# Performance work log

Measured on AMD Instinct MI355X. Metric: run time of the kernel, lower is better.

The kernel has to match this reference:

```python
import jax, jax.numpy as jnp
import numpy as np

N_NODES = 100000
N_EDGES = 1600000
N_IN = 64
N_OUT = 64


def setup_inputs() -> dict:
    key = jax.random.key(0)
    k_x, k_w, k_src, k_dst, k_val = jax.random.split(key, 5)
    X = jax.random.normal(k_x, (N_NODES, N_IN), dtype=jnp.float32)
    # Xavier-uniform init of the GCN weight matrix
    limit = float(np.sqrt(6.0 / (N_IN + N_OUT)))
    W = jax.random.uniform(k_w, (N_IN, N_OUT), dtype=jnp.float32,
                           minval=-limit, maxval=limit)
    # Sparse adjacency A in COO form: out[dst] += val * h[src]
    edge_src = jax.random.randint(k_src, (N_EDGES,), 0, N_NODES, dtype=jnp.int32)
    edge_dst = jax.random.randint(k_dst, (N_EDGES,), 0, N_NODES, dtype=jnp.int32)
    # normalized adjacency values (e.g., 1/sqrt(d_i d_j)); use uniform(0,1)
    edge_val = jax.random.uniform(k_val, (N_EDGES,), dtype=jnp.float32)
    return {"X": X, "W": W, "edge_val": edge_val,
            "edge_src": edge_src, "edge_dst": edge_dst}


def reference(X, W, edge_val, edge_src, edge_dst):
    # dropout p=0.0 -> identity (eval-mode math)
    h = X @ W                                   # [N, n_out] feature transform
    msgs = h[edge_src] * edge_val[:, None]      # [E, n_out] gather + scale
    agg = jax.ops.segment_sum(msgs, edge_dst, num_segments=N_NODES)  # A @ h
    return jax.nn.relu(agg)
```

## Files before the change

kernel.cpp:

```cpp
#include <hip/hip_runtime.h>
#include <hip/hip_bf16.h>

#define N_NODES 100000
#define N_IN    64
#define N_OUT   64
#define N_EDGES 1600000

#define BSHIFT  7
#define NPB     128
#define NB      782
#define CAP     2560
#define P1_EPT  32
#define P1_EPB  (512 * P1_EPT)
#define P1_BLOCKS ((N_EDGES + P1_EPB - 1) / P1_EPB)
#define GEMM_BLOCKS ((N_NODES + 63) / 64)

__device__ inline unsigned short f2bf(float f) {
    __hip_bfloat16 b = __float2bfloat16(f);
    union { __hip_bfloat16 b; unsigned short u; } c; c.b = b; return c.u;
}

__global__ __launch_bounds__(512) void prep_kernel(
        const float* __restrict__ X, const float* __restrict__ W,
        unsigned short* __restrict__ h,
        const int* __restrict__ edge_src, const int* __restrict__ edge_dst,
        const float* __restrict__ edge_val,
        int* __restrict__ bucket_cursor, int2* __restrict__ staged) {
    __shared__ float Ws[N_IN * N_OUT];
    const int t = threadIdx.x;

    if (blockIdx.x >= P1_BLOCKS) {
        const int blk = blockIdx.x - P1_BLOCKS;
        for (int i = t * 4; i < N_IN * N_OUT; i += 512 * 4)
            *(float4*)&Ws[i] = *(const float4*)&W[i];
        __syncthreads();

        const int r0 = blk * 64 + (t >> 4) * 2;
        const int c0 = (t & 15) * 4;
        if (r0 >= N_NODES) return;

        float acc0[4] = {0.f, 0.f, 0.f, 0.f};
        float acc1[4] = {0.f, 0.f, 0.f, 0.f};
        const float* x0p = X + (size_t)r0 * N_IN;
        const float* x1p = x0p + N_IN;

#pragma unroll 4
        for (int k4 = 0; k4 < 16; ++k4) {
            const float4 x0 = *(const float4*)(x0p + k4 * 4);
            const float4 x1 = *(const float4*)(x1p + k4 * 4);
            const float xa0[4] = {x0.x, x0.y, x0.z, x0.w};
            const float xa1[4] = {x1.x, x1.y, x1.z, x1.w};
#pragma unroll
            for (int kk = 0; kk < 4; ++kk) {
                const float4 w = *(const float4*)&Ws[(k4 * 4 + kk) * N_OUT + c0];
                acc0[0] = fmaf(xa0[kk], w.x, acc0[0]);
                acc0[1] = fmaf(xa0[kk], w.y, acc0[1]);
                acc0[2] = fmaf(xa0[kk], w.z, acc0[2]);
                acc0[3] = fmaf(xa0[kk], w.w, acc0[3]);
                acc1[0] = fmaf(xa1[kk], w.x, acc1[0]);
                acc1[1] = fmaf(xa1[kk], w.y, acc1[1]);
                acc1[2] = fmaf(xa1[kk], w.z, acc1[2]);
                acc1[3] = fmaf(xa1[kk], w.w, acc1[3]);
            }
        }
        ushort4 s0 = {f2bf(acc0[0]), f2bf(acc0[1]), f2bf(acc0[2]), f2bf(acc0[3])};
        ushort4 s1 = {f2bf(acc1[0]), f2bf(acc1[1]), f2bf(acc1[2]), f2bf(acc1[3])};
        *(ushort4*)&h[(size_t)r0 * N_OUT + c0] = s0;
        *(ushort4*)&h[(size_t)(r0 + 1) * N_OUT + c0] = s1;
    } else {
        int* cnt  = (int*)Ws;
        int* base = cnt + NB;
        for (int i = t; i < NB; i += 512) cnt[i] = 0;
        __syncthreads();

        const int e0 = blockIdx.x * P1_EPB + t * P1_EPT;
        const bool act = (e0 + P1_EPT) <= N_EDGES;

        if (act) {
#pragma unroll
            for (int q = 0; q < P1_EPT / 4; ++q) {
                const int4 d4 = *(const int4*)(edge_dst + e0 + q * 4);
                atomicAdd(&cnt[d4.x >> BSHIFT], 1);
                atomicAdd(&cnt[d4.y >> BSHIFT], 1);
                atomicAdd(&cnt[d4.z >> BSHIFT], 1);
                atomicAdd(&cnt[d4.w >> BSHIFT], 1);
            }
        }
        __syncthreads();
        for (int i = t; i < NB; i += 512) {
            const int c = cnt[i];
            base[i] = c ? atomicAdd(&bucket_cursor[i], c) : 0;
            cnt[i] = 0;
        }
        __syncthreads();
        if (act) {
#pragma unroll
            for (int q = 0; q < P1_EPT / 4; ++q) {
                const int4 d4 = *(const int4*)(edge_dst + e0 + q * 4);
                const int4 s4 = *(const int4*)(edge_src + e0 + q * 4);
                const int4 v4 = *(const int4*)((const int*)edge_val + e0 + q * 4);
                const int da[4] = {d4.x, d4.y, d4.z, d4.w};
                const int sa[4] = {s4.x, s4.y, s4.z, s4.w};
                const int va[4] = {v4.x, v4.y, v4.z, v4.w};
#pragma unroll
                for (int j = 0; j < 4; ++j) {
                    const int d = da[j];
                    const int b = d >> BSHIFT;
                    const int r = atomicAdd(&cnt[b], 1);
                    const int pos = base[b] + r;
                    if (pos < CAP) {
                        int2 o;
                        o.x = sa[j] | ((d & (NPB - 1)) << 17);
                        o.y = va[j];
                        staged[(size_t)b * CAP + pos] = o;
                    }
                }
            }
        }
    }
}

__global__ __launch_bounds__(512) void sort_gather_kernel(
        const uint2* __restrict__ h64,
        const int2* __restrict__ staged,
        const int* __restrict__ bucket_cursor,
        float* __restrict__ out) {
    __shared__ int2 srt[CAP];
    __shared__ int  ncnt[NPB];
    __shared__ int  noff[NPB];
    const int t = threadIdx.x;
    const int b = blockIdx.x;
    const int cnt = min(bucket_cursor[b], CAP);
    const int2* bucket = staged + (size_t)b * CAP;

    if (t < NPB) ncnt[t] = 0;
    __syncthreads();
    for (int e = t; e < cnt; e += 512)
        atomicAdd(&ncnt[(unsigned)bucket[e].x >> 17], 1);
    __syncthreads();
    if (t < NPB) noff[t] = ncnt[t];
    __syncthreads();
    for (int d = 1; d < NPB; d <<= 1) {
        int x = 0;
        if (t < NPB && t >= d) x = noff[t - d];
        __syncthreads();
        if (t < NPB) noff[t] += x;
        __syncthreads();
    }
    if (t < NPB) {
        const int excl = noff[t] - ncnt[t];
        noff[t] = excl;
        ncnt[t] = excl;
    }
    __syncthreads();
    for (int e = t; e < cnt; e += 512) {
        const int2 p = bucket[e];
        const int node = (unsigned)p.x >> 17;
        const int pos = atomicAdd(&ncnt[node], 1);
        int2 o; o.x = p.x & 0x1FFFF; o.y = p.y;
        srt[pos] = o;
    }
    __syncthreads();

    const int w  = t >> 6;
    const int q  = (t >> 4) & 3;
    const int ql = t & 15;

#define EDGE4(p, hw, v)                                                     \
    do {                                                                    \
        a0 = fmaf(__uint_as_float((hw).x << 16), (v), a0);                  \
        a1 = fmaf(__uint_as_float((hw).x & 0xffff0000u), (v), a1);          \
        a2 = fmaf(__uint_as_float((hw).y << 16), (v), a2);                  \
        a3 = fmaf(__uint_as_float((hw).y & 0xffff0000u), (v), a3);          \
    } while (0)

    for (int nl = w * 16; nl < w * 16 + 16; ++nl) {
        const int node = b * NPB + nl;
        if (node >= N_NODES) break;
        const int s = noff[nl];
        const int e_end = ncnt[nl];

        float a0 = 0.f, a1 = 0.f, a2 = 0.f, a3 = 0.f;
        int e = s + q;
        for (; e + 4 < e_end; e += 8) {
            const int2 p0 = srt[e];
            const int2 p1 = srt[e + 4];
            const uint2 w0 = h64[(size_t)p0.x * 16 + ql];
            const uint2 w1 = h64[(size_t)p1.x * 16 + ql];
            const float v0 = __int_as_float(p0.y);
            const float v1 = __int_as_float(p1.y);
            EDGE4(p0, w0, v0);
            EDGE4(p1, w1, v1);
        }
        for (; e < e_end; e += 4) {
            const int2 p = srt[e];
            const uint2 w0 = h64[(size_t)p.x * 16 + ql];
            const float v = __int_as_float(p.y);
            EDGE4(p, w0, v);
        }
        a0 += __shfl_xor(a0, 16, 64); a0 += __shfl_xor(a0, 32, 64);
        a1 += __shfl_xor(a1, 16, 64); a1 += __shfl_xor(a1, 32, 64);
        a2 += __shfl_xor(a2, 16, 64); a2 += __shfl_xor(a2, 32, 64);
        a3 += __shfl_xor(a3, 16, 64); a3 += __shfl_xor(a3, 32, 64);
        if (q == 0) {
            float4 o;
            o.x = fmaxf(a0, 0.f);
            o.y = fmaxf(a1, 0.f);
            o.z = fmaxf(a2, 0.f);
            o.w = fmaxf(a3, 0.f);
            *(float4*)&out[(size_t)node * 64 + 4 * ql] = o;
        }
    }
#undef EDGE4
}

__global__ __launch_bounds__(256) void gemm_f32_kernel(const float* __restrict__ X,
                                                       const float* __restrict__ W,
                                                       float* __restrict__ h) {
    __shared__ float Ws[N_IN * N_OUT];
    for (int i = threadIdx.x * 4; i < N_IN * N_OUT; i += 256 * 4)
        *(float4*)&Ws[i] = *(const float4*)&W[i];
    __syncthreads();
    const int lane = threadIdx.x & 63;
    const int wid = threadIdx.x >> 6;
    for (int row = blockIdx.x * 4 + wid; row < N_NODES; row += gridDim.x * 4) {
        const float x = X[row * N_IN + lane];
        float acc = 0.0f;
#pragma unroll
        for (int k = 0; k < N_IN; ++k)
            acc = fmaf(__shfl(x, k), Ws[k * N_OUT + lane], acc);
        h[row * N_OUT + lane] = acc;
    }
}

__global__ __launch_bounds__(256) void scatter_kernel(const float* __restrict__ h,
                                                      const float* __restrict__ edge_val,
                                                      const int* __restrict__ edge_src,
                                                      const int* __restrict__ edge_dst,
                                                      float* __restrict__ out) {
    const int lane = threadIdx.x & 63;
    const int e = (int)((blockIdx.x * 256u + threadIdx.x) >> 6);
    if (e >= N_EDGES) return;
    const float m = h[(size_t)edge_src[e] * N_OUT + lane] * edge_val[e];
    atomicAdd(&out[(size_t)edge_dst[e] * N_OUT + lane], m);
}

__global__ __launch_bounds__(256) void relu_kernel(float* __restrict__ out, int n) {
    const int i = (int)(blockIdx.x * 256u + threadIdx.x) * 4;
    if (i + 3 < n) {
        float4 v = *(float4*)&out[i];
        v.x = fmaxf(v.x, 0.f); v.y = fmaxf(v.y, 0.f);
        v.z = fmaxf(v.z, 0.f); v.w = fmaxf(v.w, 0.f);
        *(float4*)&out[i] = v;
    }
}

extern "C" void kernel_launch(void* const* d_in, const int* in_sizes, int n_in,
                              void* d_out, int out_size, void* d_ws, size_t ws_size,
                              hipStream_t stream) {
    const float* X        = (const float*)d_in[0];
    const float* W        = (const float*)d_in[1];
    const float* edge_val = (const float*)d_in[2];
    const int*   edge_src = (const int*)d_in[3];
    const int*   edge_dst = (const int*)d_in[4];
    float*       out      = (float*)d_out;

    unsigned short* h   = (unsigned short*)d_ws;
    int2* staged        = (int2*)((char*)d_ws + (size_t)N_NODES * N_OUT * 2);
    int*  bucket_cursor = (int*)(staged + (size_t)NB * CAP);
    const size_t need = (size_t)((char*)(bucket_cursor + NB) - (char*)d_ws);

    if (ws_size >= need) {
        hipMemsetAsync(bucket_cursor, 0, NB * sizeof(int), stream);
        prep_kernel<<<P1_BLOCKS + GEMM_BLOCKS, 512, 0, stream>>>(
            X, W, h, edge_src, edge_dst, edge_val, bucket_cursor, staged);
        sort_gather_kernel<<<NB, 512, 0, stream>>>((const uint2*)h, staged,
                                                   bucket_cursor, out);
    } else {
        float* hf = (float*)d_ws;
        hipMemsetAsync(d_out, 0, (size_t)out_size * sizeof(float), stream);
        gemm_f32_kernel<<<25000, 256, 0, stream>>>(X, W, hf);
        const long long st = (long long)N_EDGES * 64;
        scatter_kernel<<<(int)((st + 255) / 256), 256, 0, stream>>>(
            hf, edge_val, edge_src, edge_dst, out);
        relu_kernel<<<(out_size / 4 + 255) / 256, 256, 0, stream>>>(out, out_size);
    }
}
```

Baseline: 174.2 us.

## Stage edges in shared memory by bucket before coalesced global scatter

The binning pass now does a local counting sort in LDS. It prefix-scans the per-bucket counts and places each edge's packed (src, dst-low, val) record into a shared buffer ordered by bucket. Each wavefront then copies contiguous bucket runs to the global staged array, replacing scattered 8-byte writes with mostly contiguous ones. Edges per thread are halved so a block's edges fit in LDS, at the cost of more blocks, more global cursor atomics, a ~100KB LDS footprint that limits occupancy, and extra scan barriers.

```diff
diff --git a/kernel.cpp b/kernel.cpp
--- a/kernel.cpp
+++ b/kernel.cpp
@@ -10,10 +10,18 @@
 #define NPB     128
 #define NB      782
 #define CAP     2560
-#define P1_EPT  32
+#define P1_EPT  16
 #define P1_EPB  (512 * P1_EPT)
 #define P1_BLOCKS ((N_EDGES + P1_EPB - 1) / P1_EPB)
 #define GEMM_BLOCKS ((N_NODES + 63) / 64)
+
+#define SMEM_BYTES 100480
+#define OFF_SED   0
+#define OFF_LSCAN 65536
+#define OFF_CNT   69632
+#define OFF_GBASE 72760
+#define OFF_BKT   75888
+#define OFF_DLOW  92272
 
 __device__ inline unsigned short f2bf(float f) {
     __hip_bfloat16 b = __float2bfloat16(f);
@@ -26,10 +34,11 @@
         const int* __restrict__ edge_src, const int* __restrict__ edge_dst,
         const float* __restrict__ edge_val,
         int* __restrict__ bucket_cursor, int2* __restrict__ staged) {
-    __shared__ float Ws[N_IN * N_OUT];
+    __shared__ __align__(16) char smem[SMEM_BYTES];
     const int t = threadIdx.x;
 
     if (blockIdx.x >= P1_BLOCKS) {
+        float* Ws = (float*)smem;
         const int blk = blockIdx.x - P1_BLOCKS;
         for (int i = t * 4; i < N_IN * N_OUT; i += 512 * 4)
             *(float4*)&Ws[i] = *(const float4*)&W[i];
@@ -68,8 +77,13 @@
         *(ushort4*)&h[(size_t)r0 * N_OUT + c0] = s0;
         *(ushort4*)&h[(size_t)(r0 + 1) * N_OUT + c0] = s1;
     } else {
-        int* cnt  = (int*)Ws;
-        int* base = cnt + NB;
+        int2*           sed   = (int2*)(smem + OFF_SED);
+        int*            lscan = (int*)(smem + OFF_LSCAN);
+        int*            cnt   = (int*)(smem + OFF_CNT);
+        int*            gbase = (int*)(smem + OFF_GBASE);
+        unsigned short* bkt   = (unsigned short*)(smem + OFF_BKT);
+        unsigned char*  dlw   = (unsigned char*)(smem + OFF_DLOW);
+
         for (int i = t; i < NB; i += 512) cnt[i] = 0;
         __syncthreads();
 
@@ -80,41 +94,72 @@
 #pragma unroll
             for (int q = 0; q < P1_EPT / 4; ++q) {
                 const int4 d4 = *(const int4*)(edge_dst + e0 + q * 4);
-                atomicAdd(&cnt[d4.x >> BSHIFT], 1);
-                atomicAdd(&cnt[d4.y >> BSHIFT], 1);
-                atomicAdd(&cnt[d4.z >> BSHIFT], 1);
-                atomicAdd(&cnt[d4.w >> BSHIFT], 1);
+                const int da[4] = {d4.x, d4.y, d4.z, d4.w};
+#pragma unroll
+                for (int j = 0; j < 4; ++j) {
+                    const int k = t * P1_EPT + q * 4 + j;
+                    const int d = da[j];
+                    const int b = d >> BSHIFT;
+                    bkt[k] = (unsigned short)b;
+                    dlw[k] = (unsigned char)(d & (NPB - 1));
+                    atomicAdd(&cnt[b], 1);
+                }
             }
         }
         __syncthreads();
+
+        lscan[t]       = (t < NB) ? cnt[t] : 0;
+        lscan[t + 512] = (t + 512 < NB) ? cnt[t + 512] : 0;
+        __syncthreads();
+#pragma unroll
+        for (int dd = 1; dd < 1024; dd <<= 1) {
+            const int a0 = (t >= dd) ? lscan[t - dd] : 0;
+            const int a1 = lscan[t + 512 - dd];
+            __syncthreads();
+            lscan[t] += a0;
+            lscan[t + 512] += a1;
+            __syncthreads();
+        }
         for (int i = t; i < NB; i += 512) {
             const int c = cnt[i];
-            base[i] = c ? atomicAdd(&bucket_cursor[i], c) : 0;
+            lscan[i] -= c;
+            gbase[i] = c ? atomicAdd(&bucket_cursor[i], c) : 0;
             cnt[i] = 0;
         }
         __syncthreads();
+
         if (act) {
 #pragma unroll
             for (int q = 0; q < P1_EPT / 4; ++q) {
-                const int4 d4 = *(const int4*)(edge_dst + e0 + q * 4);
                 const int4 s4 = *(const int4*)(edge_src + e0 + q * 4);
                 const int4 v4 = *(const int4*)((const int*)edge_val + e0 + q * 4);
-                const int da[4] = {d4.x, d4.y, d4.z, d4.w};
                 const int sa[4] = {s4.x, s4.y, s4.z, s4.w};
                 const int va[4] = {v4.x, v4.y, v4.z, v4.w};
 #pragma unroll
                 for (int j = 0; j < 4; ++j) {
-                    const int d = da[j];
-                    const int b = d >> BSHIFT;
+                    const int k = t * P1_EPT + q * 4 + j;
+                    const int b = bkt[k];
                     const int r = atomicAdd(&cnt[b], 1);
-                    const int pos = base[b] + r;
-                    if (pos < CAP) {
-                        int2 o;
-                        o.x = sa[j] | ((d & (NPB - 1)) << 17);
-                        o.y = va[j];
-                        staged[(size_t)b * CAP + pos] = o;
-                    }
+                    int2 o;
+                    o.x = sa[j] | ((int)dlw[k] << 17);
+                    o.y = va[j];
+                    sed[lscan[b] + r] = o;
                 }
+            }
+        }
+        __syncthreads();
+
+        const int wv = t >> 6, lane = t & 63;
+        for (int bb = wv; bb < NB; bb += 8) {
+            const int c  = cnt[bb];
+            if (c == 0) continue;
+            const int st = lscan[bb];
+            const int g0 = gbase[bb];
+            const int2* sp = sed + st;
+            int2* dp = staged + (size_t)bb * CAP;
+            for (int k = lane; k < c; k += 64) {
+                const int pos = g0 + k;
+                if (pos < CAP) dp[pos] = sp[k];
             }
         }
     }
```

After: 174.2 us. No clear change (-0.0%).

## Locally sort edges by bucket in shared memory before coalesced staging writes

Applied to the files above, without the earlier changes.

Splits the combined prep kernel into a separate bucketing kernel and GEMM kernel. The bucketing kernel now counts each 8192-edge chunk per bucket, prefix-scans the counts, scatters edges into a shared-memory buffer grouped by bucket, and then has each wave copy contiguous runs to the global staged array. This replaces scattered 8-byte global writes with mostly contiguous ones. In exchange it uses about 90KB of shared memory per block, which limits occupancy, adds an extra kernel launch, and removes the overlap between GEMM and bucketing blocks.

```diff
diff --git a/kernel.cpp b/kernel.cpp
--- a/kernel.cpp
+++ b/kernel.cpp
@@ -10,9 +10,8 @@
 #define NPB     128
 #define NB      782
 #define CAP     2560
-#define P1_EPT  32
-#define P1_EPB  (512 * P1_EPT)
-#define P1_BLOCKS ((N_EDGES + P1_EPB - 1) / P1_EPB)
+#define EPB     8192
+#define BKT_BLOCKS ((N_EDGES + EPB - 1) / EPB)
 #define GEMM_BLOCKS ((N_NODES + 63) / 64)
 
 __device__ inline unsigned short f2bf(float f) {
@@ -20,104 +19,152 @@
     union { __hip_bfloat16 b; unsigned short u; } c; c.b = b; return c.u;
 }
 
-__global__ __launch_bounds__(512) void prep_kernel(
-        const float* __restrict__ X, const float* __restrict__ W,
-        unsigned short* __restrict__ h,
+__global__ __launch_bounds__(512) void bucket_kernel(
         const int* __restrict__ edge_src, const int* __restrict__ edge_dst,
         const float* __restrict__ edge_val,
         int* __restrict__ bucket_cursor, int2* __restrict__ staged) {
+    __shared__ int2           sed[EPB];
+    __shared__ int            cnt[NB];
+    __shared__ int            lstart[NB];
+    __shared__ int            gbase[NB];
+    __shared__ unsigned short bkt[EPB];
+    __shared__ unsigned char  dlw[EPB];
+    __shared__ int            wtot[8], woff[8];
+
+    const int t = threadIdx.x;
+    const int lane = t & 63, wv = t >> 6;
+    const int B0 = blockIdx.x * EPB;
+
+    for (int i = t; i < NB; i += 512) cnt[i] = 0;
+    __syncthreads();
+
+#pragma unroll
+    for (int q = 0; q < 4; ++q) {
+        const int e = B0 + q * 2048 + t * 4;
+        if (e + 4 <= N_EDGES) {
+            const int4 d4 = *(const int4*)(edge_dst + e);
+            const int da[4] = {d4.x, d4.y, d4.z, d4.w};
+            const int k = q * 2048 + t * 4;
+#pragma unroll
+            for (int j = 0; j < 4; ++j) {
+                const int d = da[j];
+                bkt[k + j] = (unsigned short)(d >> BSHIFT);
+                dlw[k + j] = (unsigned char)(d & (NPB - 1));
+                atomicAdd(&cnt[d >> BSHIFT], 1);
+            }
+        }
+    }
+    __syncthreads();
+
+    const int i0 = 2 * t, i1 = 2 * t + 1;
+    const int c0 = (i0 < NB) ? cnt[i0] : 0;
+    const int c1 = (i1 < NB) ? cnt[i1] : 0;
+    int incl = c0 + c1;
+#pragma unroll
+    for (int d = 1; d < 64; d <<= 1) {
+        const int o = __shfl_up(incl, d, 64);
+        if (lane >= d) incl += o;
+    }
+    if (lane == 63) wtot[wv] = incl;
+    __syncthreads();
+    if (t < 8) {
+        int v = wtot[t];
+        int vincl = v;
+#pragma unroll
+        for (int d = 1; d < 8; d <<= 1) {
+            const int o = __shfl_up(vincl, d, 8);
+            if (t >= d) vincl += o;
+        }
+        woff[t] = vincl - v;
+    }
+    __syncthreads();
+    const int ebase = woff[wv] + (incl - (c0 + c1));
+    if (i0 < NB) lstart[i0] = ebase;
+    if (i1 < NB) lstart[i1] = ebase + c0;
+    for (int i = t; i < NB; i += 512) {
+        const int c = cnt[i];
+        gbase[i] = c ? atomicAdd(&bucket_cursor[i], c) : 0;
+        cnt[i] = 0;
+    }
+    __syncthreads();
+
+#pragma unroll
+    for (int q = 0; q < 4; ++q) {
+        const int e = B0 + q * 2048 + t * 4;
+        if (e + 4 <= N_EDGES) {
+            const int4 s4 = *(const int4*)(edge_src + e);
+            const int4 v4 = *(const int4*)((const int*)edge_val + e);
+            const int sa[4] = {s4.x, s4.y, s4.z, s4.w};
+            const int va[4] = {v4.x, v4.y, v4.z, v4.w};
+            const int k = q * 2048 + t * 4;
+#pragma unroll
+            for (int j = 0; j < 4; ++j) {
+                const int b = bkt[k + j];
+                const int r = atomicAdd(&cnt[b], 1);
+                int2 o;
+                o.x = sa[j] | ((int)dlw[k + j] << 17);
+                o.y = va[j];
+                sed[lstart[b] + r] = o;
+            }
+        }
+    }
+    __syncthreads();
+
+    for (int bb = wv; bb < NB; bb += 8) {
+        const int c = cnt[bb];
+        if (c == 0) continue;
+        const int st = lstart[bb];
+        const int g0 = gbase[bb];
+        const int2* sp = sed + st;
+        int2* dp = staged + (size_t)bb * CAP;
+        for (int k = lane; k < c; k += 64) {
+            const int pos = g0 + k;
+            if (pos < CAP) dp[pos] = sp[k];
+        }
+    }
+}
+
+__global__ __launch_bounds__(512) void gemm_kernel(
+        const float* __restrict__ X, const float* __restrict__ W,
+        unsigned short* __restrict__ h) {
     __shared__ float Ws[N_IN * N_OUT];
     const int t = threadIdx.x;
-
-    if (blockIdx.x >= P1_BLOCKS) {
-        const int blk = blockIdx.x - P1_BLOCKS;
-        for (int i = t * 4; i < N_IN * N_OUT; i += 512 * 4)
-            *(float4*)&Ws[i] = *(const float4*)&W[i];
-        __syncthreads();
-
-        const int r0 = blk * 64 + (t >> 4) * 2;
-        const int c0 = (t & 15) * 4;
-        if (r0 >= N_NODES) return;
-
-        float acc0[4] = {0.f, 0.f, 0.f, 0.f};
-        float acc1[4] = {0.f, 0.f, 0.f, 0.f};
-        const float* x0p = X + (size_t)r0 * N_IN;
-        const float* x1p = x0p + N_IN;
+    for (int i = t * 4; i < N_IN * N_OUT; i += 512 * 4)
+        *(float4*)&Ws[i] = *(const float4*)&W[i];
+    __syncthreads();
+
+    const int r0 = blockIdx.x * 64 + (t >> 4) * 2;
+    const int c0 = (t & 15) * 4;
+    if (r0 >= N_NODES) return;
+
+    float acc0[4] = {0.f, 0.f, 0.f, 0.f};
+    float acc1[4] = {0.f, 0.f, 0.f, 0.f};
+    const float* x0p = X + (size_t)r0 * N_IN;
+    const float* x1p = x0p + N_IN;
 
 #pragma unroll 4
-        for (int k4 = 0; k4 < 16; ++k4) {
-            const float4 x0 = *(const float4*)(x0p + k4 * 4);
-            const float4 x1 = *(const float4*)(x1p + k4 * 4);
-            const float xa0[4] = {x0.x, x0.y, x0.z, x0.w};
-            const float xa1[4] = {x1.x, x1.y, x1.z, x1.w};
-#pragma unroll
-            for (int kk = 0; kk < 4; ++kk) {
-                const float4 w = *(const float4*)&Ws[(k4 * 4 + kk) * N_OUT + c0];
-                acc0[0] = fmaf(xa0[kk], w.x, acc0[0]);
-                acc0[1] = fmaf(xa0[kk], w.y, acc0[1]);
-                acc0[2] = fmaf(xa0[kk], w.z, acc0[2]);
-                acc0[3] = fmaf(xa0[kk], w.w, acc0[3]);
-                acc1[0] = fmaf(xa1[kk], w.x, acc1[0]);
-                acc1[1] = fmaf(xa1[kk], w.y, acc1[1]);
-                acc1[2] = fmaf(xa1[kk], w.z, acc1[2]);
-                acc1[3] = fmaf(xa1[kk], w.w, acc1[3]);
-            }
-        }
-        ushort4 s0 = {f2bf(acc0[0]), f2bf(acc0[1]), f2bf(acc0[2]), f2bf(acc0[3])};
-        ushort4 s1 = {f2bf(acc1[0]), f2bf(acc1[1]), f2bf(acc1[2]), f2bf(acc1[3])};
-        *(ushort4*)&h[(size_t)r0 * N_OUT + c0] = s0;
-        *(ushort4*)&h[(size_t)(r0 + 1) * N_OUT + c0] = s1;
-    } else {
-        int* cnt  = (int*)Ws;
-        int* base = cnt + NB;
-        for (int i = t; i < NB; i += 512) cnt[i] = 0;
-        __syncthreads();
-
-        const int e0 = blockIdx.x * P1_EPB + t * P1_EPT;
-        const bool act = (e0 + P1_EPT) <= N_EDGES;
-
-        if (act) {
-#pragma unroll
-            for (int q = 0; q < P1_EPT / 4; ++q) {
-                const int4 d4 = *(const int4*)(edge_dst + e0 + q * 4);
-                atomicAdd(&cnt[d4.x >> BSHIFT], 1);
-                atomicAdd(&cnt[d4.y >> BSHIFT], 1);
-                atomicAdd(&cnt[d4.z >> BSHIFT], 1);
-                atomicAdd(&cnt[d4.w >> BSHIFT], 1);
-            }
-        }
-        __syncthreads();
-        for (int i = t; i < NB; i += 512) {
-            const int c = cnt[i];
-            base[i] = c ? atomicAdd(&bucket_cursor[i], c) : 0;
-            cnt[i] = 0;
-        }
-        __syncthreads();
-        if (act) {
-#pragma unroll
-            for (int q = 0; q < P1_EPT / 4; ++q) {
-                const int4 d4 = *(const int4*)(edge_dst + e0 + q * 4);
-                const int4 s4 = *(const int4*)(edge_src + e0 + q * 4);
-                const int4 v4 = *(const int4*)((const int*)edge_val + e0 + q * 4);
-                const int da[4] = {d4.x, d4.y, d4.z, d4.w};
-                const int sa[4] = {s4.x, s4.y, s4.z, s4.w};
-                const int va[4] = {v4.x, v4.y, v4.z, v4.w};
-#pragma unroll
-                for (int j = 0; j < 4; ++j) {
-                    const int d = da[j];
-                    const int b = d >> BSHIFT;
-                    const int r = atomicAdd(&cnt[b], 1);
-                    const int pos = base[b] + r;
-                    if (pos < CAP) {
-                        int2 o;
-                        o.x = sa[j] | ((d & (NPB - 1)) << 17);
-                        o.y = va[j];
-                        staged[(size_t)b * CAP + pos] = o;
-                    }
-                }
-            }
-        }
-    }
+    for (int k4 = 0; k4 < 16; ++k4) {
+        const float4 x0 = *(const float4*)(x0p + k4 * 4);
+        const float4 x1 = *(const float4*)(x1p + k4 * 4);
+        const float xa0[4] = {x0.x, x0.y, x0.z, x0.w};
+        const float xa1[4] = {x1.x, x1.y, x1.z, x1.w};
+#pragma unroll
+        for (int kk = 0; kk < 4; ++kk) {
+            const float4 w = *(const float4*)&Ws[(k4 * 4 + kk) * N_OUT + c0];
+            acc0[0] = fmaf(xa0[kk], w.x, acc0[0]);
+            acc0[1] = fmaf(xa0[kk], w.y, acc0[1]);
+            acc0[2] = fmaf(xa0[kk], w.z, acc0[2]);
+            acc0[3] = fmaf(xa0[kk], w.w, acc0[3]);
+            acc1[0] = fmaf(xa1[kk], w.x, acc1[0]);
+            acc1[1] = fmaf(xa1[kk], w.y, acc1[1]);
+            acc1[2] = fmaf(xa1[kk], w.z, acc1[2]);
+            acc1[3] = fmaf(xa1[kk], w.w, acc1[3]);
+        }
+    }
+    ushort4 s0 = {f2bf(acc0[0]), f2bf(acc0[1]), f2bf(acc0[2]), f2bf(acc0[3])};
+    ushort4 s1 = {f2bf(acc1[0]), f2bf(acc1[1]), f2bf(acc1[2]), f2bf(acc1[3])};
+    *(ushort4*)&h[(size_t)r0 * N_OUT + c0] = s0;
+    *(ushort4*)&h[(size_t)(r0 + 1) * N_OUT + c0] = s1;
 }
 
 __global__ __launch_bounds__(512) void sort_gather_kernel(
@@ -272,8 +319,9 @@
 
     if (ws_size >= need) {
         hipMemsetAsync(bucket_cursor, 0, NB * sizeof(int), stream);
-        prep_kernel<<<P1_BLOCKS + GEMM_BLOCKS, 512, 0, stream>>>(
-            X, W, h, edge_src, edge_dst, edge_val, bucket_cursor, staged);
+        bucket_kernel<<<BKT_BLOCKS, 512, 0, stream>>>(
+            edge_src, edge_dst, edge_val, bucket_cursor, staged);
+        gemm_kernel<<<GEMM_BLOCKS, 512, 0, stream>>>(X, W, h);
         sort_gather_kernel<<<NB, 512, 0, stream>>>((const uint2*)h, staged,
                                                    bucket_cursor, out);
     } else {
```

After: 172.1 us. About the same (-1.2%).
